# Optimization experiments

Hardware: AMD Instinct MI355X
Metric: run time of the kernel (lower is better)

The kernel has to match this reference:

```python
import jax, jax.numpy as jnp
import numpy as np

N, D = 2097152, 10  # tokens, feature dim (pinned by nn.Linear(10,10))


def setup_inputs() -> dict:
    key = jax.random.key(0)
    kx, kr, kw1, kb1, kw2, kb2 = jax.random.split(key, 6)
    s = 1.0 / np.sqrt(D)  # torch nn.Linear default init range
    x = jax.random.normal(kx, (N, D), dtype=jnp.float32)
    route = jax.random.randint(kr, (N,), 0, 2, dtype=jnp.int32)  # RandScatter decision
    W1 = jax.random.uniform(kw1, (D, D), jnp.float32, -s, s)
    b1 = jax.random.uniform(kb1, (D,), jnp.float32, -s, s)
    W2 = jax.random.uniform(kw2, (D, D), jnp.float32, -s, s)
    b2 = jax.random.uniform(kb2, (D,), jnp.float32, -s, s)
    return {"x": x, "W1": W1, "b1": b1, "W2": W2, "b2": b2, "route": route}


def reference(x, W1, b1, W2, b2, route):
    # Original: scatter rows by `route` to expert1/expert2 (Linear 10->10),
    # then gather back to original row order. Equivalent dense form:
    # out[i] = expert_{route[i]}(x[i]). The 10x10 GEMMs are negligible, so
    # computing both branches and selecting is the efficient vectorized form.
    y0 = x @ W1.T + b1  # [N, D] expert1 on all rows
    y1 = x @ W2.T + b2  # [N, D] expert2 on all rows
    return jnp.where((route == 0)[:, None], y0, y1)
```

## Files before the change

### kernel.cpp

```cpp
#include <hip/hip_runtime.h>


#define BLOCK 256
#define D 10
#define WAVE_ROWS 128
#define F4_PER_WAVE 320
#define ROWS_PER_BLOCK 512

typedef float f4 __attribute__((ext_vector_type(4)));
typedef float f2 __attribute__((ext_vector_type(2)));

__global__ __launch_bounds__(BLOCK) void moe_kernel(
    const float* __restrict__ x,
    const float* __restrict__ W1,
    const float* __restrict__ b1,
    const float* __restrict__ W2,
    const float* __restrict__ b2,
    const int*   __restrict__ route,
    float*       __restrict__ out,
    int n)
{
    __shared__ f4 lds[(BLOCK / 64) * F4_PER_WAVE];

    const int lane = threadIdx.x & 63;
    const int wave = threadIdx.x >> 6;
    f4* __restrict__ wlds = lds + wave * F4_PER_WAVE;

    const long long rowbase =
        ((long long)blockIdx.x * (BLOCK / 64) + wave) * WAVE_ROWS;

    if (rowbase + WAVE_ROWS <= n) {
        const f4* __restrict__ xv = (const f4*)(x + rowbase * D);
        f4 bx[5];
        #pragma unroll
        for (int j = 0; j < 5; ++j)
            bx[j] = xv[j * 64 + lane];
        const int2 rt = ((const int2*)(route + rowbase))[lane];

        #pragma unroll
        for (int j = 0; j < 5; ++j)
            wlds[j * 64 + lane] = bx[j];
        __builtin_amdgcn_wave_barrier();

        float xf[2 * D];
        #pragma unroll
        for (int j = 0; j < 5; ++j) {
            f4 t = wlds[lane * 5 + j];
            xf[4 * j + 0] = t.x; xf[4 * j + 1] = t.y;
            xf[4 * j + 2] = t.z; xf[4 * j + 3] = t.w;
        }

        f2 xp[D];
        #pragma unroll
        for (int k = 0; k < D; ++k)
            xp[k] = (f2){xf[k], xf[D + k]};

        float o0[D], o1[D];
        #pragma unroll
        for (int j = 0; j < D; ++j) {
            f2 a0 = (f2){b1[j], b1[j]};
            f2 a1 = (f2){b2[j], b2[j]};
            #pragma unroll
            for (int k = 0; k < D; ++k) {
                const float w1 = W1[j * D + k];
                const float w2 = W2[j * D + k];
                a0 = __builtin_elementwise_fma(xp[k], (f2){w1, w1}, a0);
                a1 = __builtin_elementwise_fma(xp[k], (f2){w2, w2}, a1);
            }
            o0[j] = rt.x ? a1.x : a0.x;
            o1[j] = rt.y ? a1.y : a0.y;
        }

        __builtin_amdgcn_wave_barrier();
        {
            f4 t0 = (f4){o0[0], o0[1], o0[2], o0[3]};
            f4 t1 = (f4){o0[4], o0[5], o0[6], o0[7]};
            f4 t2 = (f4){o0[8], o0[9], o1[0], o1[1]};
            f4 t3 = (f4){o1[2], o1[3], o1[4], o1[5]};
            f4 t4 = (f4){o1[6], o1[7], o1[8], o1[9]};
            wlds[lane * 5 + 0] = t0;
            wlds[lane * 5 + 1] = t1;
            wlds[lane * 5 + 2] = t2;
            wlds[lane * 5 + 3] = t3;
            wlds[lane * 5 + 4] = t4;
        }
        __builtin_amdgcn_wave_barrier();

        f4* __restrict__ ov = (f4*)(out + rowbase * D);
        #pragma unroll
        for (int j = 0; j < 5; ++j) {
            f4 t = wlds[j * 64 + lane];
            __builtin_nontemporal_store(t, &ov[j * 64 + lane]);
        }
    } else {
        for (int r = 0; r < 2; ++r) {
            const long long row = rowbase + lane * 2 + r;
            if (row < n) {
                const int sel = route[row];
                for (int j = 0; j < D; ++j) {
                    float y0 = b1[j];
                    float y1 = b2[j];
                    for (int k = 0; k < D; ++k) {
                        const float xk = x[row * D + k];
                        y0 = fmaf(xk, W1[j * D + k], y0);
                        y1 = fmaf(xk, W2[j * D + k], y1);
                    }
                    out[row * D + j] = sel ? y1 : y0;
                }
            }
        }
    }
}

extern "C" void kernel_launch(void* const* d_in, const int* in_sizes, int n_in,
                              void* d_out, int out_size, void* d_ws, size_t ws_size,
                              hipStream_t stream) {
    const float* x     = (const float*)d_in[0];
    const float* W1    = (const float*)d_in[1];
    const float* b1    = (const float*)d_in[2];
    const float* W2    = (const float*)d_in[3];
    const float* b2    = (const float*)d_in[4];
    const int*   route = (const int*)d_in[5];
    float*       out   = (float*)d_out;

    const int n = in_sizes[5];
    const int blocks = (n + ROWS_PER_BLOCK - 1) / ROWS_PER_BLOCK;

    moe_kernel<<<blocks, BLOCK, 0, stream>>>(x, W1, b1, W2, b2, route, out, n);
}
```

Measured before the change: 163.9 us.

## Load x and route directly into LDS and process two chunks per wave

Replaces the register-staged global loads with global_load_lds that copies x and route straight into LDS, and gives each wave two 128-row chunks. Explicit vmcnt waits let compute on the first chunk start while the second chunk is still loading, and all stores are deferred until both chunks finish. The block shrinks to 128 threads. This aims to cut VGPR use and the LDS write pass and to raise memory-level parallelism, but it relies on hand-counted vmcnt values and leaves a stray label in the code.

```diff
diff --git a/kernel.cpp b/kernel.cpp
--- a/kernel.cpp
+++ b/kernel.cpp
@@ -1,14 +1,22 @@
 #include <hip/hip_runtime.h>
 
 
-#define BLOCK 256
+#define BLOCK 128
 #define D 10
-#define WAVE_ROWS 128
-#define F4_PER_WAVE 320
-#define ROWS_PER_BLOCK 512
+#define CHUNK_ROWS 128
+#define NCHUNK 2
+#define ROWS_PER_WAVE (CHUNK_ROWS * NCHUNK)
+#define WAVES_PER_BLOCK (BLOCK / 64)
+#define ROWS_PER_BLOCK (ROWS_PER_WAVE * WAVES_PER_BLOCK)
+#define F4_PER_CHUNK 320
 
 typedef float f4 __attribute__((ext_vector_type(4)));
 typedef float f2 __attribute__((ext_vector_type(2)));
+
+#define GLL16(gsrc, ldst)                                                   \
+    __builtin_amdgcn_global_load_lds(                                       \
+        (const __attribute__((address_space(1))) void*)(gsrc),              \
+        (__attribute__((address_space(3))) void*)(ldst), 16, 0, 0)
 
 __global__ __launch_bounds__(BLOCK) void moe_kernel(
     const float* __restrict__ x,
@@ -20,81 +28,109 @@
     float*       __restrict__ out,
     int n)
 {
-    __shared__ f4 lds[(BLOCK / 64) * F4_PER_WAVE];
+    __shared__ f4  xbuf[WAVES_PER_BLOCK][NCHUNK][F4_PER_CHUNK];
+    __shared__ int rbuf[WAVES_PER_BLOCK][ROWS_PER_WAVE];
 
     const int lane = threadIdx.x & 63;
     const int wave = threadIdx.x >> 6;
-    f4* __restrict__ wlds = lds + wave * F4_PER_WAVE;
+    f4*  __restrict__ xb0 = xbuf[wave][0];
+    f4*  __restrict__ xb1 = xbuf[wave][1];
+    int* __restrict__ rb  = rbuf[wave];
 
-    const long long rowbase =
-        ((long long)blockIdx.x * (BLOCK / 64) + wave) * WAVE_ROWS;
+    const long long wavebase =
+        ((long long)blockIdx.x * WAVES_PER_BLOCK + wave) * ROWS_PER_WAVE;
 
-    if (rowbase + WAVE_ROWS <= n) {
-        const f4* __restrict__ xv = (const f4*)(x + rowbase * D);
-        f4 bx[5];
+    if (wavebase + ROWS_PER_WAVE <= n) {
+        GLL16(route + wavebase + 4 * lane, rb);
+        const float* xs0 = x + wavebase * D;
+        const float* xs1 = x + (wavebase + CHUNK_ROWS) * D;
         #pragma unroll
         for (int j = 0; j < 5; ++j)
-            bx[j] = xv[j * 64 + lane];
-        const int2 rt = ((const int2*)(route + rowbase))[lane];
+            GLL16(xs0 + j * 256 + 4 * lane, xb0 + j * 64);
+        #pragma unroll
+        for (int j = 0; j < 5; ++j)
+            GLL16(xs1 + j * 256 + 4 * lane, xb1 + j * 64);
+
+        f4 st0[5], st1[5];
 
         #pragma unroll
-        for (int j = 0; j < 5; ++j)
-            wlds[j * 64 + lane] = bx[j];
-        __builtin_amdgcn_wave_barrier();
+        for (int p = 0; p < NCHUNK; ++p) {
+            f4* __restrict__ xb = p ? xb1 : xb0;
 
-        float xf[2 * D];
-        #pragma unroll
-        for (int j = 0; j < 5; ++j) {
-            f4 t = wlds[lane * 5 + j];
-            xf[4 * j + 0] = t.x; xf[4 * j + 1] = t.y;
-            xf[4 * j + 2] = t.z; xf[4 * j + 3] = t.w;
+            if (p == 0) {
+                asm volatile("s_waitcnt vmcnt(5)" ::: "memory");
+            } else {
+                asm volatile("s_waitcnt vmcnt(0)" ::: "memory");
+            }
+            __builtin_amdgcn_sched_barrier(0);
+
+            float xf[2 * D];
+            #pragma unroll
+            for (int j = 0; j < 5; ++j) {
+                f4 t = xb[lane * 5 + j];
+                xf[4 * j + 0] = t.x; xf[4 * j + 1] = t.y;
+                xf[4 * j + 2] = t.z; xf[4 * j + 3] = t.w;
+            }
+            const int2 rt = *(const int2*)(rb + p * CHUNK_ROWS + 2 * lane);
+
+            f2 xp[D];
+            #pragma unroll
+            for (int k = 0; k < D; ++k)
+                xp[k] = (f2){xf[k], xf[D + k]};
+
+            float o0[D], o1[D];
+            #pragma unroll
+            for (int j = 0; j < D; ++j) {
+                f2 a0 = (f2){b1[j], b1[j]};
+                f2 a1 = (f2){b2[j], b2[j]};
+                #pragma unroll
+                for (int k = 0; k < D; ++k) {
+                    const float w1 = W1[j * D + k];
+                    const float w2 = W2[j * D + k];
+                    a0 = __builtin_elementwise_fma(xp[k], (f2){w1, w1}, a0);
+                    a1 = __builtin_elementwise_fma(xp[k], (f2){w2, w2}, a1);
+                }
+                o0[j] = rt.x ? a1.x : a0.x;
+                o1[j] = rt.y ? a1.y : a0.y;
+            }
+
+            __builtin_amdgcn_wave_barrier();
+            {
+                wlds_write:
+                f4 t0 = (f4){o0[0], o0[1], o0[2], o0[3]};
+                f4 t1 = (f4){o0[4], o0[5], o0[6], o0[7]};
+                f4 t2 = (f4){o0[8], o0[9], o1[0], o1[1]};
+                f4 t3 = (f4){o1[2], o1[3], o1[4], o1[5]};
+                f4 t4 = (f4){o1[6], o1[7], o1[8], o1[9]};
+                xb[lane * 5 + 0] = t0;
+                xb[lane * 5 + 1] = t1;
+                xb[lane * 5 + 2] = t2;
+                xb[lane * 5 + 3] = t3;
+                xb[lane * 5 + 4] = t4;
+            }
+            __builtin_amdgcn_wave_barrier();
+
+            f4* st = p ? st1 : st0;
+            #pragma unroll
+            for (int j = 0; j < 5; ++j)
+                st[j] = xb[j * 64 + lane];
+            if (p == 1) break;
         }
 
-        f2 xp[D];
-        #pragma unroll
-        for (int k = 0; k < D; ++k)
-            xp[k] = (f2){xf[k], xf[D + k]};
-
-        float o0[D], o1[D];
-        #pragma unroll
-        for (int j = 0; j < D; ++j) {
-            f2 a0 = (f2){b1[j], b1[j]};
-            f2 a1 = (f2){b2[j], b2[j]};
+        {
+            f4* __restrict__ ov0 = (f4*)(out + wavebase * D);
+            f4* __restrict__ ov1 = (f4*)(out + (wavebase + CHUNK_ROWS) * D);
             #pragma unroll
-            for (int k = 0; k < D; ++k) {
-                const float w1 = W1[j * D + k];
-                const float w2 = W2[j * D + k];
-                a0 = __builtin_elementwise_fma(xp[k], (f2){w1, w1}, a0);
-                a1 = __builtin_elementwise_fma(xp[k], (f2){w2, w2}, a1);
-            }
-            o0[j] = rt.x ? a1.x : a0.x;
-            o1[j] = rt.y ? a1.y : a0.y;
-        }
-
-        __builtin_amdgcn_wave_barrier();
-        {
-            f4 t0 = (f4){o0[0], o0[1], o0[2], o0[3]};
-            f4 t1 = (f4){o0[4], o0[5], o0[6], o0[7]};
-            f4 t2 = (f4){o0[8], o0[9], o1[0], o1[1]};
-            f4 t3 = (f4){o1[2], o1[3], o1[4], o1[5]};
-            f4 t4 = (f4){o1[6], o1[7], o1[8], o1[9]};
-            wlds[lane * 5 + 0] = t0;
-            wlds[lane * 5 + 1] = t1;
-            wlds[lane * 5 + 2] = t2;
-            wlds[lane * 5 + 3] = t3;
-            wlds[lane * 5 + 4] = t4;
-        }
-        __builtin_amdgcn_wave_barrier();
-
-        f4* __restrict__ ov = (f4*)(out + rowbase * D);
-        #pragma unroll
-        for (int j = 0; j < 5; ++j) {
-            f4 t = wlds[j * 64 + lane];
-            __builtin_nontemporal_store(t, &ov[j * 64 + lane]);
+            for (int j = 0; j < 5; ++j)
+                __builtin_nontemporal_store(st0[j], &ov0[j * 64 + lane]);
+            #pragma unroll
+            for (int j = 0; j < 5; ++j)
+                __builtin_nontemporal_store(st1[j], &ov1[j * 64 + lane]);
         }
     } else {
-        for (int r = 0; r < 2; ++r) {
-            const long long row = rowbase + lane * 2 + r;
+        for (int r = 0; r < ROWS_PER_WAVE / 64; ++r) {
+            const long long row =
+                wavebase + (long long)lane * (ROWS_PER_WAVE / 64) + r;
             if (row < n) {
                 const int sel = route[row];
                 for (int j = 0; j < D; ++j) {
```

Result: no change. 166.3 us (+1.5%).
